# Optimization experiments

Measured on AMD Instinct MI355X. Metric: run time of the kernel, lower is better.

Reference implementation:

```python
import jax, jax.numpy as jnp
import numpy as np

B, S, H = 1, 2048, 1024
NQ, NKV, HD = 16, 8, 64
FF, E, TOPK = 2048, 4, 2
WINDOW = 512
CAP = 50.0
CLIP_L, CLIP_R = -0.03, 1.03
EPS = 1e-5
ROPE_BASE = 10000.0


def setup_inputs() -> dict:
    key = jax.random.key(0)
    ks = jax.random.split(key, 14)
    std = 0.02
    def nrm(k, shape):
        return jax.random.normal(k, shape, jnp.float32) * std
    return {
        'x': jax.random.normal(ks[0], (B, S, H), jnp.float32),
        'norm1_w': 1.0 + nrm(ks[1], (H,)),
        'wq': nrm(ks[2], (H, NQ * HD)),
        'wk': nrm(ks[3], (H, NKV * HD)),
        'wv': nrm(ks[4], (H, NKV * HD)),
        'wo': nrm(ks[5], (NQ * HD, H)),
        'qn_w': 1.0 + nrm(ks[6], (HD,)),
        'kn_w': 1.0 + nrm(ks[7], (HD,)),
        'norm2_w': 1.0 + nrm(ks[8], (H,)),
        'gate_w': nrm(ks[9], (H, E)),
        'w_gate': nrm(ks[10], (E, H, FF)),
        'w_up': nrm(ks[11], (E, H, FF)),
        'w_down': nrm(ks[12], (E, FF, H)),
    }


def _rms(x, w):
    return x * jax.lax.rsqrt(jnp.mean(x * x, axis=-1, keepdims=True) + EPS) * w


def _rope(t):
    # t: [B, S, N, D]
    D = t.shape[-1]
    half = D // 2
    inv = 1.0 / (ROPE_BASE ** (jnp.arange(half, dtype=jnp.float32) / half))
    ang = jnp.arange(t.shape[1], dtype=jnp.float32)[:, None] * inv  # [S, half]
    cos = jnp.cos(ang)[None, :, None, :]
    sin = jnp.sin(ang)[None, :, None, :]
    t1, t2 = t[..., :half], t[..., half:]
    return jnp.concatenate([t1 * cos - t2 * sin, t1 * sin + t2 * cos], axis=-1)


def reference(x, norm1_w, wq, wk, wv, wo, qn_w, kn_w, norm2_w, gate_w, w_gate, w_up, w_down):
    # --- self-attention block ---
    xn = _rms(x, norm1_w)
    q = (xn @ wq).reshape(B, S, NQ, HD)
    k = (xn @ wk).reshape(B, S, NKV, HD)
    v = (xn @ wv).reshape(B, S, NKV, HD)
    q = _rms(_rope(q), qn_w)  # RoPE then QK-norm over head_dim
    k = _rms(_rope(k), kn_w)
    rep = NQ // NKV
    k = jnp.repeat(k, rep, axis=2)  # GQA expand to NQ heads
    v = jnp.repeat(v, rep, axis=2)
    scale = 1.0 / np.sqrt(HD).astype(np.float32)
    scores = jnp.einsum('bqhd,bkhd->bhqk', q, k) * scale
    scores = CAP * jnp.tanh(scores / CAP)  # softmax capping (overrides temperature)
    i = jnp.arange(S)[:, None]
    j = jnp.arange(S)[None, :]
    allow = (j <= i) & (i - j < WINDOW)  # causal + sliding window
    scores = jnp.where(allow[None, None], scores, -jnp.inf)
    p = jax.nn.softmax(scores, axis=-1)
    p = jnp.clip((CLIP_R - CLIP_L) * p + CLIP_L, 0.0, 1.0)  # softmax clipping
    attn = jnp.einsum('bhqk,bkhd->bqhd', p, v).reshape(B, S, NQ * HD)
    h = x + attn @ wo
    # --- MoE gated-SiLU MLP block ---
    xn2 = _rms(h, norm2_w).reshape(B * S, H)
    probs = jax.nn.softmax(xn2 @ gate_w, axis=-1)
    topv, topi = jax.lax.top_k(probs, TOPK)
    topv = topv / jnp.sum(topv, axis=-1, keepdims=True)
    T = B * S
    wdense = jnp.zeros((T, E), jnp.float32).at[jnp.arange(T)[:, None], topi].add(topv)
    g = jnp.einsum('th,ehf->etf', xn2, w_gate)
    u = jnp.einsum('th,ehf->etf', xn2, w_up)
    y = jnp.einsum('etf,efh->eth', jax.nn.silu(g) * u, w_down)
    moe = jnp.einsum('eth,te->th', y, wdense)
    return h + moe.reshape(B, S, H)
```

## Files before the change

kernel.cpp:

```cpp
#include <hip/hip_runtime.h>
#include <hip/hip_bf16.h>
#include <math.h>

#define S_LEN   2048
#define H_DIM   1024
#define N_QH    16
#define N_KVH   8
#define HEADD   64
#define FF_DIM  2048
#define N_EXP   4
#define WIN     512
#define QB      16
#define SCS     596

typedef __attribute__((ext_vector_type(8))) short bf16x8;
typedef __attribute__((ext_vector_type(4))) float f32x4;

__device__ __forceinline__ short f2bf(float x) {
  unsigned u = __float_as_uint(x);
  u += 0x7fffu + ((u >> 16) & 1u);
  return (short)(u >> 16);
}
__device__ __forceinline__ float bf2f(short h) {
  return __uint_as_float((unsigned)(unsigned short)h << 16);
}
__device__ __forceinline__ unsigned pk2(short a, short b) {
  return (unsigned)(unsigned short)a | ((unsigned)(unsigned short)b << 16);
}
__device__ __forceinline__ int swz(int row, int col) {
  return row * 64 + (col ^ ((row & 7) << 3));
}

__global__ __launch_bounds__(256) void k_rope_tables(float* __restrict__ ct, float* __restrict__ st) {
  int i = blockIdx.x * 256 + threadIdx.x;
  int t = i >> 5, d = i & 31;
  double inv = 1.0 / pow(10000.0, (double)d / 32.0);
  double ang = (double)t * inv;
  ct[i] = (float)cos(ang);
  st[i] = (float)sin(ang);
}

template <int MODE>
__global__ __launch_bounds__(256) void k_rmsnorm(const float* __restrict__ x,
                                                 const float* __restrict__ w,
                                                 short* __restrict__ yh,
                                                 short* __restrict__ yl,
                                                 const float* __restrict__ gw,
                                                 float* __restrict__ wd) {
  int row = blockIdx.x;
  const float4 v = ((const float4*)(x + (long)row * H_DIM))[threadIdx.x];
  float ss = v.x * v.x + v.y * v.y + v.z * v.z + v.w * v.w;
  for (int off = 32; off; off >>= 1) ss += __shfl_xor(ss, off);
  __shared__ float red[4];
  if ((threadIdx.x & 63) == 0) red[threadIdx.x >> 6] = ss;
  __syncthreads();
  ss = red[0] + red[1] + red[2] + red[3];
  float r = (float)(1.0 / sqrt((double)ss * (1.0 / 1024.0) + 1e-5));
  const float4 wv = ((const float4*)w)[threadIdx.x];
  float4 o;
  o.x = v.x * r * wv.x; o.y = v.y * r * wv.y; o.z = v.z * r * wv.z; o.w = v.w * r * wv.w;
  if (MODE == 2) {
    short h0 = f2bf(o.x), h1 = f2bf(o.y), h2 = f2bf(o.z), h3 = f2bf(o.w);
    short l0 = f2bf(o.x - bf2f(h0)), l1 = f2bf(o.y - bf2f(h1));
    short l2 = f2bf(o.z - bf2f(h2)), l3 = f2bf(o.w - bf2f(h3));
    ((uint2*)(yh + (long)row * H_DIM))[threadIdx.x] = make_uint2(pk2(h0, h1), pk2(h2, h3));
    ((uint2*)(yl + (long)row * H_DIM))[threadIdx.x] = make_uint2(pk2(l0, l1), pk2(l2, l3));
  }
  if (MODE == 3) {
    ((uint2*)(yh + (long)row * H_DIM))[threadIdx.x] =
        make_uint2(pk2(f2bf(o.x), f2bf(o.y)), pk2(f2bf(o.z), f2bf(o.w)));
    int i0 = threadIdx.x * 4;
    float4 g0 = *(const float4*)&gw[(i0 + 0) * 4];
    float4 g1 = *(const float4*)&gw[(i0 + 1) * 4];
    float4 g2 = *(const float4*)&gw[(i0 + 2) * 4];
    float4 g3 = *(const float4*)&gw[(i0 + 3) * 4];
    float p0 = o.x * g0.x + o.y * g1.x + o.z * g2.x + o.w * g3.x;
    float p1 = o.x * g0.y + o.y * g1.y + o.z * g2.y + o.w * g3.y;
    float p2 = o.x * g0.z + o.y * g1.z + o.z * g2.z + o.w * g3.z;
    float p3 = o.x * g0.w + o.y * g1.w + o.z * g2.w + o.w * g3.w;
    for (int off = 32; off; off >>= 1) {
      p0 += __shfl_xor(p0, off); p1 += __shfl_xor(p1, off);
      p2 += __shfl_xor(p2, off); p3 += __shfl_xor(p3, off);
    }
    __shared__ float gred[4][4];
    int wid = threadIdx.x >> 6;
    if ((threadIdx.x & 63) == 0) { gred[wid][0] = p0; gred[wid][1] = p1; gred[wid][2] = p2; gred[wid][3] = p3; }
    __syncthreads();
    if (threadIdx.x == 0) {
      float l[4];
      for (int e = 0; e < 4; ++e) l[e] = gred[0][e] + gred[1][e] + gred[2][e] + gred[3][e];
      int i1 = 0;
      for (int e = 1; e < 4; ++e) if (l[e] > l[i1]) i1 = e;
      int i2 = -1;
      for (int e = 0; e < 4; ++e) { if (e == i1) continue; if (i2 < 0 || l[e] > l[i2]) i2 = e; }
      float e2 = expf(l[i2] - l[i1]);
      float w1 = 1.f / (1.f + e2);
      float ov[4] = {0.f, 0.f, 0.f, 0.f};
      ov[i1] = w1; ov[i2] = 1.f - w1;
      wd[row * 4 + 0] = ov[0]; wd[row * 4 + 1] = ov[1];
      wd[row * 4 + 2] = ov[2]; wd[row * 4 + 3] = ov[3];
    }
  }
}

__global__ __launch_bounds__(256) void k_tsplit(const float* __restrict__ in,
                                                short* __restrict__ oh,
                                                short* __restrict__ ol, int R, int C) {
  __shared__ float tile[32][33];
  int bx = blockIdx.x, by = blockIdx.y;
  int lx = threadIdx.x & 31, ly = threadIdx.x >> 5;
  int xc = bx * 32 + lx;
#pragma unroll
  for (int k = 0; k < 4; ++k) {
    int y = by * 32 + ly + k * 8;
    tile[ly + k * 8][lx] = in[(long)y * C + xc];
  }
  __syncthreads();
  int ox = by * 32 + lx;
#pragma unroll
  for (int k = 0; k < 4; ++k) {
    int oy = bx * 32 + ly + k * 8;
    float v = tile[lx][ly + k * 8];
    short hb = f2bf(v);
    short lb = f2bf(v - bf2f(hb));
    oh[(long)oy * R + ox] = hb;
    ol[(long)oy * R + ox] = lb;
  }
}

__global__ __launch_bounds__(256) void k_transpose_cast(const float* __restrict__ in,
                                                        short* __restrict__ out,
                                                        int R, int C) {
  __shared__ float tile[32][33];
  int bx = blockIdx.x, by = blockIdx.y;
  int lx = threadIdx.x & 31, ly = threadIdx.x >> 5;
  int x = bx * 32 + lx;
#pragma unroll
  for (int k = 0; k < 4; ++k) {
    int y = by * 32 + ly + k * 8;
    tile[ly + k * 8][lx] = in[(long)y * C + x];
  }
  __syncthreads();
  int ox = by * 32 + lx;
#pragma unroll
  for (int k = 0; k < 4; ++k) {
    int oy = bx * 32 + ly + k * 8;
    out[(long)oy * R + ox] = f2bf(tile[lx][ly + k * 8]);
  }
}

template <int ADD>
__global__ __launch_bounds__(256) void k_gemm_split(const short* __restrict__ Ah,
                                                    const short* __restrict__ Al,
                                                    const short* __restrict__ Bh,
                                                    const short* __restrict__ Bl,
                                                    const float* __restrict__ R,
                                                    float* __restrict__ C,
                                                    int K, int ldA, int ldB, int ldC) {
  __shared__ short AsH[128 * 64], AsL[128 * 64], BsH[128 * 64], BsL[128 * 64];
  const int r0 = blockIdx.x * 128, c0 = blockIdx.y * 128;
  const int tid = threadIdx.x;
  const int wid = tid >> 6, lane = tid & 63;
  const int wr = wid >> 1, wc = wid & 1;
  const int lr = lane & 15, lg = lane >> 4;
  f32x4 zero = {0.f, 0.f, 0.f, 0.f};
  f32x4 acc[4][4];
#pragma unroll
  for (int m = 0; m < 4; ++m)
#pragma unroll
    for (int n = 0; n < 4; ++n) acc[m][n] = zero;
  for (int k0 = 0; k0 < K; k0 += 64) {
#pragma unroll
    for (int it = 0; it < 4; ++it) {
      int flat = tid + it * 256;
      int row = flat >> 3, cb = (flat & 7) * 8;
      int d = swz(row, cb);
      *(uint4*)&AsH[d] = *(const uint4*)&Ah[(long)(r0 + row) * ldA + k0 + cb];
      *(uint4*)&AsL[d] = *(const uint4*)&Al[(long)(r0 + row) * ldA + k0 + cb];
      *(uint4*)&BsH[d] = *(const uint4*)&Bh[(long)(c0 + row) * ldB + k0 + cb];
      *(uint4*)&BsL[d] = *(const uint4*)&Bl[(long)(c0 + row) * ldB + k0 + cb];
    }
    __syncthreads();
#pragma unroll
    for (int kk = 0; kk < 64; kk += 32) {
      bf16x8 ah[4], al[4], bh[4], bl[4];
#pragma unroll
      for (int m = 0; m < 4; ++m) {
        int d = swz(wr * 64 + m * 16 + lr, kk + lg * 8);
        ah[m] = *(const bf16x8*)&AsH[d];
        al[m] = *(const bf16x8*)&AsL[d];
      }
#pragma unroll
      for (int n = 0; n < 4; ++n) {
        int d = swz(wc * 64 + n * 16 + lr, kk + lg * 8);
        bh[n] = *(const bf16x8*)&BsH[d];
        bl[n] = *(const bf16x8*)&BsL[d];
      }
#pragma unroll
      for (int m = 0; m < 4; ++m)
#pragma unroll
        for (int n = 0; n < 4; ++n) {
          acc[m][n] = __builtin_amdgcn_mfma_f32_16x16x32_bf16(ah[m], bh[n], acc[m][n], 0, 0, 0);
          acc[m][n] = __builtin_amdgcn_mfma_f32_16x16x32_bf16(ah[m], bl[n], acc[m][n], 0, 0, 0);
          acc[m][n] = __builtin_amdgcn_mfma_f32_16x16x32_bf16(al[m], bh[n], acc[m][n], 0, 0, 0);
        }
    }
    __syncthreads();
  }
#pragma unroll
  for (int m = 0; m < 4; ++m)
#pragma unroll
    for (int n = 0; n < 4; ++n) {
      int col = c0 + wc * 64 + n * 16 + lr;
#pragma unroll
      for (int r = 0; r < 4; ++r) {
        int row = r0 + wr * 64 + m * 16 + lg * 4 + r;
        float v = acc[m][n][r];
        if (ADD) v += R[(long)row * ldC + col];
        C[(long)row * ldC + col] = v;
      }
    }
}

__global__ __launch_bounds__(256) void k_rope_rms(float* __restrict__ qkv,
                                                  const float* __restrict__ qn_w,
                                                  const float* __restrict__ kn_w,
                                                  const float* __restrict__ ct,
                                                  const float* __restrict__ st) {
  int idx = blockIdx.x * 4 + (threadIdx.x >> 6);
  int lane = threadIdx.x & 63;
  int t = idx / 24, hh = idx - t * 24;
  long base; const float* w;
  if (hh < N_QH) { base = (long)t * 2048 + hh * HEADD;              w = qn_w; }
  else           { base = (long)t * 2048 + 1024 + (hh - N_QH) * HEADD; w = kn_w; }
  float x = qkv[base + lane];
  float partner = __shfl_xor(x, 32);
  int d = lane & 31;
  float cs = ct[t * 32 + d], sn = st[t * 32 + d];
  float r = x * cs + partner * ((lane < 32) ? -sn : sn);
  float ss = r * r;
  for (int off = 32; off; off >>= 1) ss += __shfl_xor(ss, off);
  float rr = (float)(1.0 / sqrt((double)ss * (1.0 / 64.0) + 1e-5));
  qkv[base + lane] = r * rr * w[lane];
}

__global__ __launch_bounds__(256) void k_kv_split(const float* __restrict__ qkv,
                                                  short* __restrict__ Kbh, short* __restrict__ Kbl,
                                                  short* __restrict__ Vth, short* __restrict__ Vtl) {
  const int kvh = blockIdx.y;
  const int jb = blockIdx.x * 64;
  const int tid = threadIdx.x;
  {
    int j = jb + (tid >> 2);
    int dq = (tid & 3) * 16;
    const float* kp = &qkv[(long)j * 2048 + 1024 + kvh * HEADD + dq];
    long ob = ((long)kvh * S_LEN + j) * HEADD + dq;
#pragma unroll
    for (int u4 = 0; u4 < 4; ++u4) {
      float4 f = *(const float4*)&kp[u4 * 4];
      short h0 = f2bf(f.x), h1 = f2bf(f.y), h2 = f2bf(f.z), h3 = f2bf(f.w);
      short l0 = f2bf(f.x - bf2f(h0)), l1 = f2bf(f.y - bf2f(h1));
      short l2 = f2bf(f.z - bf2f(h2)), l3 = f2bf(f.w - bf2f(h3));
      *(uint2*)&Kbh[ob + u4 * 4] = make_uint2(pk2(h0, h1), pk2(h2, h3));
      *(uint2*)&Kbl[ob + u4 * 4] = make_uint2(pk2(l0, l1), pk2(l2, l3));
    }
  }
  {
    int d = tid & 63;
    int j0 = jb + (tid >> 6) * 16;
    short hb[16], lb[16];
#pragma unroll
    for (int u = 0; u < 16; ++u) {
      float f = qkv[(long)(j0 + u) * 2048 + 1536 + kvh * HEADD + d];
      hb[u] = f2bf(f);
      lb[u] = f2bf(f - bf2f(hb[u]));
    }
    long ob = ((long)kvh * HEADD + d) * S_LEN + j0;
#pragma unroll
    for (int w = 0; w < 2; ++w) {
      uint4 oh, ol;
      oh.x = pk2(hb[w * 8 + 0], hb[w * 8 + 1]); oh.y = pk2(hb[w * 8 + 2], hb[w * 8 + 3]);
      oh.z = pk2(hb[w * 8 + 4], hb[w * 8 + 5]); oh.w = pk2(hb[w * 8 + 6], hb[w * 8 + 7]);
      ol.x = pk2(lb[w * 8 + 0], lb[w * 8 + 1]); ol.y = pk2(lb[w * 8 + 2], lb[w * 8 + 3]);
      ol.z = pk2(lb[w * 8 + 4], lb[w * 8 + 5]); ol.w = pk2(lb[w * 8 + 6], lb[w * 8 + 7]);
      *(uint4*)&Vth[ob + w * 8] = oh;
      *(uint4*)&Vtl[ob + w * 8] = ol;
    }
  }
}

__global__ __launch_bounds__(256) void k_attn2(const float* __restrict__ qkv,
                                               const short* __restrict__ Kbh,
                                               const short* __restrict__ Kbl,
                                               const short* __restrict__ Vth,
                                               const short* __restrict__ Vtl,
                                               short* __restrict__ attHi,
                                               short* __restrict__ attLo) {
  __shared__ float sc[QB][SCS];
  __shared__ float row_a[QB];
  const int i0 = blockIdx.x * QB;
  const int hq = blockIdx.y;
  const int kvh = hq >> 1;
  const int tid = threadIdx.x;
  const int wv = tid >> 6, lane = tid & 63;
  const int lr = lane & 15, lg = lane >> 4;
  const int jstart = (i0 >= WIN) ? ((i0 - (WIN - 1)) & ~63) : 0;
  const int nch = (i0 + QB - jstart + 63) >> 6;
  const int ncols = nch * 64;
  f32x4 zero = {0.f, 0.f, 0.f, 0.f};
  const short* Kh_p = Kbh + (long)kvh * S_LEN * HEADD;
  const short* Kl_p = Kbl + (long)kvh * S_LEN * HEADD;
  const short* Vh_p = Vth + (long)kvh * HEADD * S_LEN;
  const short* Vl_p = Vtl + (long)kvh * HEADD * S_LEN;

  bf16x8 qh[2], ql[2];
  {
    const float* qp = &qkv[(long)(i0 + lr) * 2048 + hq * HEADD];
#pragma unroll
    for (int kk = 0; kk < 2; ++kk) {
      float4 f0 = *(const float4*)&qp[kk * 32 + lg * 8];
      float4 f1 = *(const float4*)&qp[kk * 32 + lg * 8 + 4];
      float ff[8] = {f0.x, f0.y, f0.z, f0.w, f1.x, f1.y, f1.z, f1.w};
      bf16x8 h, l;
#pragma unroll
      for (int u = 0; u < 8; ++u) {
        short hb = f2bf(ff[u]);
        h[u] = hb; l[u] = f2bf(ff[u] - bf2f(hb));
      }
      qh[kk] = h; ql[kk] = l;
    }
  }

  for (int ch = 0; ch < nch; ++ch) {
    int jb = jstart + ch * 64;
    int jrow = jb + wv * 16 + lr;
    int jc = min(jrow, S_LEN - 1);
    f32x4 s = zero;
#pragma unroll
    for (int kk = 0; kk < 2; ++kk) {
      bf16x8 kh = *(const bf16x8*)&Kh_p[(long)jc * HEADD + kk * 32 + lg * 8];
      bf16x8 kl = *(const bf16x8*)&Kl_p[(long)jc * HEADD + kk * 32 + lg * 8];
      s = __builtin_amdgcn_mfma_f32_16x16x32_bf16(qh[kk], kh, s, 0, 0, 0);
      s = __builtin_amdgcn_mfma_f32_16x16x32_bf16(qh[kk], kl, s, 0, 0, 0);
      s = __builtin_amdgcn_mfma_f32_16x16x32_bf16(ql[kk], kh, s, 0, 0, 0);
    }
    int col = ch * 64 + wv * 16 + lr;
#pragma unroll
    for (int r = 0; r < 4; ++r) {
      int q = 4 * lg + r;
      int i = i0 + q;
      float v = s[r] * 0.125f;
      v = 50.f * tanhf(v * 0.02f);
      bool allow = (jrow <= i) && (i - jrow < WIN);
      sc[q][col] = allow ? v : -1e30f;
    }
  }
  __syncthreads();

  for (int r = wv * 4; r < wv * 4 + 4; ++r) {
    float mx = -1e30f;
    for (int n = lane; n < ncols; n += 64) mx = fmaxf(mx, sc[r][n]);
    for (int off = 32; off; off >>= 1) mx = fmaxf(mx, __shfl_xor(mx, off));
    float sum = 0.f;
    for (int n = lane; n < ncols; n += 64) {
      float p = expf(sc[r][n] - mx);
      sc[r][n] = p; sum += p;
    }
    for (int off = 32; off; off >>= 1) sum += __shfl_xor(sum, off);
    if (lane == 0) row_a[r] = 1.06f / sum;
  }
  __syncthreads();

  {
    int q = tid >> 4;
    float a = row_a[q];
    for (int n = (tid & 15); n < ncols; n += 16) {
      float e = sc[q][n];
      float p = fminf(fmaxf(fmaf(a, e, -0.03f), 0.f), 1.f);
      short ph = f2bf(p);
      short pl = f2bf(p - bf2f(ph));
      *(unsigned*)&sc[q][n] = pk2(ph, pl);
    }
  }
  __syncthreads();

  f32x4 oacc = zero;
  for (int ch = 0; ch < nch; ++ch) {
    int jb = jstart + ch * 64;
#pragma unroll
    for (int kk = 0; kk < 2; ++kk) {
      int js = jb + kk * 32 + lg * 8;
      int jcb = min(js, S_LEN - 8);
      const unsigned* pp = (const unsigned*)&sc[lr][ch * 64 + kk * 32 + lg * 8];
      uint4 w0 = *(const uint4*)&pp[0];
      uint4 w1 = *(const uint4*)&pp[4];
      bf16x8 pa, pb;
      pa[0] = (short)w0.x; pb[0] = (short)(w0.x >> 16);
      pa[1] = (short)w0.y; pb[1] = (short)(w0.y >> 16);
      pa[2] = (short)w0.z; pb[2] = (short)(w0.z >> 16);
      pa[3] = (short)w0.w; pb[3] = (short)(w0.w >> 16);
      pa[4] = (short)w1.x; pb[4] = (short)(w1.x >> 16);
      pa[5] = (short)w1.y; pb[5] = (short)(w1.y >> 16);
      pa[6] = (short)w1.z; pb[6] = (short)(w1.z >> 16);
      pa[7] = (short)w1.w; pb[7] = (short)(w1.w >> 16);
      bf16x8 vh = *(const bf16x8*)&Vh_p[(long)(wv * 16 + lr) * S_LEN + jcb];
      bf16x8 vl = *(const bf16x8*)&Vl_p[(long)(wv * 16 + lr) * S_LEN + jcb];
      oacc = __builtin_amdgcn_mfma_f32_16x16x32_bf16(pa, vh, oacc, 0, 0, 0);
      oacc = __builtin_amdgcn_mfma_f32_16x16x32_bf16(pa, vl, oacc, 0, 0, 0);
      oacc = __builtin_amdgcn_mfma_f32_16x16x32_bf16(pb, vh, oacc, 0, 0, 0);
    }
  }
#pragma unroll
  for (int r = 0; r < 4; ++r) {
    int q = 4 * lg + r;
    int d = wv * 16 + lr;
    long ob = (long)(i0 + q) * 1024 + hq * HEADD + d;
    float v = oacc[r];
    short hb = f2bf(v);
    attHi[ob] = hb;
    attLo[ob] = f2bf(v - bf2f(hb));
  }
}

template <int ATOMIC>
__global__ __launch_bounds__(256) void k_gemm_bf16(const short* __restrict__ A,
                                                   const short* __restrict__ Bt,
                                                   float* __restrict__ C,
                                                   int K, int ldA, int ldB, int ldC,
                                                   long sA, long sB, long sC) {
  __shared__ short As[128 * 64];
  __shared__ short Bs[128 * 64];
  const int e = blockIdx.z;
  A += (long)e * sA; Bt += (long)e * sB; C += (long)e * sC;
  const int r0 = blockIdx.x * 128, c0 = blockIdx.y * 128;
  const int tid = threadIdx.x;
  const int wid = tid >> 6, lane = tid & 63;
  const int wr = wid >> 1, wc = wid & 1;
  const int lr = lane & 15, lg = lane >> 4;
  f32x4 zero = {0.f, 0.f, 0.f, 0.f};
  f32x4 acc[4][4];
#pragma unroll
  for (int m = 0; m < 4; ++m)
#pragma unroll
    for (int n = 0; n < 4; ++n) acc[m][n] = zero;
  for (int k0 = 0; k0 < K; k0 += 64) {
#pragma unroll
    for (int it = 0; it < 4; ++it) {
      int flat = tid + it * 256;
      int row = flat >> 3, cb = (flat & 7) * 8;
      int d = swz(row, cb);
      *(uint4*)&As[d] = *(const uint4*)&A[(long)(r0 + row) * ldA + k0 + cb];
      *(uint4*)&Bs[d] = *(const uint4*)&Bt[(long)(c0 + row) * ldB + k0 + cb];
    }
    __syncthreads();
#pragma unroll
    for (int kk = 0; kk < 64; kk += 32) {
      bf16x8 af[4], bfr[4];
#pragma unroll
      for (int m = 0; m < 4; ++m) af[m] = *(const bf16x8*)&As[swz(wr * 64 + m * 16 + lr, kk + lg * 8)];
#pragma unroll
      for (int n = 0; n < 4; ++n) bfr[n] = *(const bf16x8*)&Bs[swz(wc * 64 + n * 16 + lr, kk + lg * 8)];
#pragma unroll
      for (int m = 0; m < 4; ++m)
#pragma unroll
        for (int n = 0; n < 4; ++n)
          acc[m][n] = __builtin_amdgcn_mfma_f32_16x16x32_bf16(af[m], bfr[n], acc[m][n], 0, 0, 0);
    }
    __syncthreads();
  }
#pragma unroll
  for (int m = 0; m < 4; ++m)
#pragma unroll
    for (int n = 0; n < 4; ++n) {
      int col = c0 + wc * 64 + n * 16 + lr;
#pragma unroll
      for (int r = 0; r < 4; ++r) {
        int row = r0 + wr * 64 + m * 16 + lg * 4 + r;
        float v = acc[m][n][r];
        if (ATOMIC) atomicAdd(&C[(long)row * ldC + col], v);
        else        C[(long)row * ldC + col] = v;
      }
    }
}

__global__ __launch_bounds__(256) void k_moe_act(const float* __restrict__ gu,
                                                 const float* __restrict__ wd,
                                                 short* __restrict__ aAll,
                                                 int e) {
  long i4 = (long)blockIdx.x * 256 + threadIdx.x;
  int t  = (int)(i4 >> 9);
  int f4 = (int)(i4 & 511);
  float wte = wd[t * 4 + e];
  float4 g = ((const float4*)gu)[(long)t * 1024 + f4];
  float4 u = ((const float4*)gu)[(long)t * 1024 + 512 + f4];
  float4 s;
  s.x = wte * u.x * g.x / (1.f + expf(-g.x));
  s.y = wte * u.y * g.y / (1.f + expf(-g.y));
  s.z = wte * u.z * g.z / (1.f + expf(-g.z));
  s.w = wte * u.w * g.w / (1.f + expf(-g.w));
  ((uint2*)(aAll + ((long)e << 22)))[i4] =
      make_uint2(pk2(f2bf(s.x), f2bf(s.y)), pk2(f2bf(s.z), f2bf(s.w)));
}

extern "C" void kernel_launch(void* const* d_in, const int* in_sizes, int n_in,
                              void* d_out, int out_size, void* d_ws, size_t ws_size,
                              hipStream_t stream) {
  const float* x       = (const float*)d_in[0];
  const float* norm1_w = (const float*)d_in[1];
  const float* wq      = (const float*)d_in[2];
  const float* wk      = (const float*)d_in[3];
  const float* wv      = (const float*)d_in[4];
  const float* wo      = (const float*)d_in[5];
  const float* qn_w    = (const float*)d_in[6];
  const float* kn_w    = (const float*)d_in[7];
  const float* norm2_w = (const float*)d_in[8];
  const float* gate_w  = (const float*)d_in[9];
  const float* w_gate  = (const float*)d_in[10];
  const float* w_up    = (const float*)d_in[11];
  const float* w_down  = (const float*)d_in[12];
  float* out = (float*)d_out;
  char* ws = (char*)d_ws;
  const unsigned long MB = 1ul << 20;

  float* ropeC = (float*)(ws + 0);
  float* ropeS = (float*)(ws + 256 * 1024);
  float* qkv   = (float*)(ws + 1 * MB);
  short* xnHi  = (short*)(ws + 17 * MB);
  short* xnLo  = (short*)(ws + 21 * MB);
  short* attHi = (short*)(ws + 25 * MB);
  short* attLo = (short*)(ws + 29 * MB);
  float* gu    = (float*)(ws + 1 * MB);
  short* qkvWh = (short*)(ws + 33 * MB);
  short* qkvWl = (short*)(ws + 37 * MB);
  short* woTh  = (short*)(ws + 41 * MB);
  short* woTl  = (short*)(ws + 43 * MB);
  float* h     = (float*)(ws + 45 * MB);
  short* guT   = (short*)(ws + 45 * MB);
  short* x2b   = (short*)(ws + 53 * MB);
  float* wd    = (float*)(ws + 57 * MB);
  short* dT    = (short*)(ws + 58 * MB);
  short* Kbh   = (short*)(ws + 58 * MB);
  short* Kbl   = (short*)(ws + 60 * MB);
  short* Vth   = (short*)(ws + 62 * MB);
  short* Vtl   = (short*)(ws + 64 * MB);
  short* aAll  = (short*)(ws + 74 * MB);

  k_rope_tables<<<256, 256, 0, stream>>>(ropeC, ropeS);
  k_rmsnorm<2><<<S_LEN, 256, 0, stream>>>(x, norm1_w, xnHi, xnLo, nullptr, nullptr);
  k_tsplit<<<dim3(32, 32), 256, 0, stream>>>(wq, qkvWh, qkvWl, 1024, 1024);
  k_tsplit<<<dim3(16, 32), 256, 0, stream>>>(wk, qkvWh + 1024 * 1024, qkvWl + 1024 * 1024, 1024, 512);
  k_tsplit<<<dim3(16, 32), 256, 0, stream>>>(wv, qkvWh + 1536 * 1024, qkvWl + 1536 * 1024, 1024, 512);
  k_tsplit<<<dim3(32, 32), 256, 0, stream>>>(wo, woTh, woTl, 1024, 1024);
  k_gemm_split<0><<<dim3(16, 16), 256, 0, stream>>>(xnHi, xnLo, qkvWh, qkvWl, nullptr, qkv,
                                                    1024, 1024, 1024, 2048);
  k_rope_rms<<<(S_LEN * 24) / 4, 256, 0, stream>>>(qkv, qn_w, kn_w, ropeC, ropeS);
  k_kv_split<<<dim3(S_LEN / 64, N_KVH), 256, 0, stream>>>(qkv, Kbh, Kbl, Vth, Vtl);
  k_attn2<<<dim3(S_LEN / QB, N_QH), 256, 0, stream>>>(qkv, Kbh, Kbl, Vth, Vtl, attHi, attLo);
  k_gemm_split<1><<<dim3(16, 8), 256, 0, stream>>>(attHi, attLo, woTh, woTl, x, h,
                                                   1024, 1024, 1024, 1024);
  k_rmsnorm<3><<<S_LEN, 256, 0, stream>>>(h, norm2_w, x2b, nullptr, gate_w, wd);
  hipMemcpyAsync(out, h, (size_t)S_LEN * H_DIM * sizeof(float), hipMemcpyDeviceToDevice, stream);
  for (int e = 0; e < N_EXP; ++e)
    k_transpose_cast<<<dim3(1024 / 32, 2048 / 32), 256, 0, stream>>>(
        w_down + (long)e * FF_DIM * H_DIM, dT + (long)e * H_DIM * FF_DIM, 2048, 1024);
  for (int e = 0; e < N_EXP; ++e) {
    k_transpose_cast<<<dim3(2048 / 32, 1024 / 32), 256, 0, stream>>>(
        w_gate + (long)e * H_DIM * FF_DIM, guT, 1024, 2048);
    k_transpose_cast<<<dim3(2048 / 32, 1024 / 32), 256, 0, stream>>>(
        w_up + (long)e * H_DIM * FF_DIM, guT + (long)FF_DIM * H_DIM, 1024, 2048);
    k_gemm_bf16<0><<<dim3(16, 32), 256, 0, stream>>>(x2b, guT, gu, 1024, 1024, 1024, 4096, 0, 0, 0);
    k_moe_act<<<4096, 256, 0, stream>>>(gu, wd, aAll, e);
  }
  k_gemm_bf16<1><<<dim3(16, 8, N_EXP), 256, 0, stream>>>(
      aAll, dT, out, 2048, 2048, 2048, 1024,
      (long)S_LEN * FF_DIM, (long)H_DIM * FF_DIM, 0);
}
```

Measured before the change: 579.7 us.

## Route MoE tokens sparsely to top-2 experts and use fast softcap/exp intrinsics

The MoE block previously ran dense GEMMs for every token through all four experts and weighted the results. A routing kernel now builds per-expert token lists with atomic counters, and the gate/up and down GEMMs gather only the assigned tokens, skipping empty tiles and scattering results with atomics. This roughly halves the MoE FLOPs, at the cost of a gather inside the A-tile load and nondeterministic token ordering. Separately, the attention tanh softcap is rewritten as an exp plus reciprocal, and expf is replaced by __expf and rcp intrinsics, trading a little precision for cheaper transcendentals.

```diff
diff --git a/kernel.cpp b/kernel.cpp
--- a/kernel.cpp
+++ b/kernel.cpp
@@ -27,6 +27,10 @@
 __device__ __forceinline__ unsigned pk2(short a, short b) {
   return (unsigned)(unsigned short)a | ((unsigned)(unsigned short)b << 16);
 }
+__device__ __forceinline__ float softcap(float s) {
+  float e = __expf(s * 0.04f);
+  return 50.f - 100.f * __builtin_amdgcn_rcpf(e + 1.f);
+}
 __device__ __forceinline__ int swz(int row, int col) {
   return row * 64 + (col ^ ((row & 7) << 3));
 }
@@ -46,7 +50,7 @@
                                                  short* __restrict__ yh,
                                                  short* __restrict__ yl,
                                                  const float* __restrict__ gw,
-                                                 float* __restrict__ wd) {
+                                                 float* __restrict__ route) {
   int row = blockIdx.x;
   const float4 v = ((const float4*)(x + (long)row * H_DIM))[threadIdx.x];
   float ss = v.x * v.x + v.y * v.y + v.z * v.z + v.w * v.w;
@@ -95,12 +99,22 @@
       for (int e = 0; e < 4; ++e) { if (e == i1) continue; if (i2 < 0 || l[e] > l[i2]) i2 = e; }
       float e2 = expf(l[i2] - l[i1]);
       float w1 = 1.f / (1.f + e2);
-      float ov[4] = {0.f, 0.f, 0.f, 0.f};
-      ov[i1] = w1; ov[i2] = 1.f - w1;
-      wd[row * 4 + 0] = ov[0]; wd[row * 4 + 1] = ov[1];
-      wd[row * 4 + 2] = ov[2]; wd[row * 4 + 3] = ov[3];
-    }
-  }
+      *(float4*)&route[row * 4] = make_float4((float)i1, (float)i2, w1, 1.f - w1);
+    }
+  }
+}
+
+__global__ __launch_bounds__(256) void k_route(const float* __restrict__ route,
+                                               int* __restrict__ idx,
+                                               float* __restrict__ wsl,
+                                               int* __restrict__ cnt) {
+  int t = blockIdx.x * 256 + threadIdx.x;
+  float4 rt = *(const float4*)&route[t * 4];
+  int e1 = (int)rt.x, e2 = (int)rt.y;
+  int s1 = atomicAdd(&cnt[e1], 1);
+  idx[e1 * S_LEN + s1] = t; wsl[e1 * S_LEN + s1] = rt.z;
+  int s2 = atomicAdd(&cnt[e2], 1);
+  idx[e2 * S_LEN + s2] = t; wsl[e2 * S_LEN + s2] = rt.w;
 }
 
 __global__ __launch_bounds__(256) void k_tsplit(const float* __restrict__ in,
@@ -349,8 +363,7 @@
     for (int r = 0; r < 4; ++r) {
       int q = 4 * lg + r;
       int i = i0 + q;
-      float v = s[r] * 0.125f;
-      v = 50.f * tanhf(v * 0.02f);
+      float v = softcap(s[r] * 0.125f);
       bool allow = (jrow <= i) && (i - jrow < WIN);
       sc[q][col] = allow ? v : -1e30f;
     }
@@ -363,7 +376,7 @@
     for (int off = 32; off; off >>= 1) mx = fmaxf(mx, __shfl_xor(mx, off));
     float sum = 0.f;
     for (int n = lane; n < ncols; n += 64) {
-      float p = expf(sc[r][n] - mx);
+      float p = __expf(sc[r][n] - mx);
       sc[r][n] = p; sum += p;
     }
     for (int off = 32; off; off >>= 1) sum += __shfl_xor(sum, off);
@@ -422,17 +435,17 @@
   }
 }
 
-template <int ATOMIC>
-__global__ __launch_bounds__(256) void k_gemm_bf16(const short* __restrict__ A,
+__global__ __launch_bounds__(256) void k_gemm_moe1(const short* __restrict__ A,
                                                    const short* __restrict__ Bt,
                                                    float* __restrict__ C,
-                                                   int K, int ldA, int ldB, int ldC,
-                                                   long sA, long sB, long sC) {
+                                                   const int* __restrict__ idx,
+                                                   const int* __restrict__ cnt) {
+  const int n = *cnt;
+  const int r0 = blockIdx.x * 128;
+  if (r0 >= n) return;
   __shared__ short As[128 * 64];
   __shared__ short Bs[128 * 64];
-  const int e = blockIdx.z;
-  A += (long)e * sA; Bt += (long)e * sB; C += (long)e * sC;
-  const int r0 = blockIdx.x * 128, c0 = blockIdx.y * 128;
+  const int c0 = blockIdx.y * 128;
   const int tid = threadIdx.x;
   const int wid = tid >> 6, lane = tid & 63;
   const int wr = wid >> 1, wc = wid & 1;
@@ -442,15 +455,82 @@
 #pragma unroll
   for (int m = 0; m < 4; ++m)
 #pragma unroll
-    for (int n = 0; n < 4; ++n) acc[m][n] = zero;
-  for (int k0 = 0; k0 < K; k0 += 64) {
+    for (int nn = 0; nn < 4; ++nn) acc[m][nn] = zero;
+  int tokRow[1];
+  for (int k0 = 0; k0 < 1024; k0 += 64) {
+#pragma unroll
+    for (int it = 0; it < 4; ++it) {
+      int flat = tid + it * 256;
+      int row = flat >> 3, cb = (flat & 7) * 8;
+      int slot = r0 + row;
+      int tok = idx[min(slot, n - 1)];
+      int d = swz(row, cb);
+      *(uint4*)&As[d] = *(const uint4*)&A[(long)tok * 1024 + k0 + cb];
+      *(uint4*)&Bs[d] = *(const uint4*)&Bt[(long)(c0 + row) * 1024 + k0 + cb];
+    }
+    (void)tokRow;
+    __syncthreads();
+#pragma unroll
+    for (int kk = 0; kk < 64; kk += 32) {
+      bf16x8 af[4], bfr[4];
+#pragma unroll
+      for (int m = 0; m < 4; ++m) af[m] = *(const bf16x8*)&As[swz(wr * 64 + m * 16 + lr, kk + lg * 8)];
+#pragma unroll
+      for (int nn = 0; nn < 4; ++nn) bfr[nn] = *(const bf16x8*)&Bs[swz(wc * 64 + nn * 16 + lr, kk + lg * 8)];
+#pragma unroll
+      for (int m = 0; m < 4; ++m)
+#pragma unroll
+        for (int nn = 0; nn < 4; ++nn)
+          acc[m][nn] = __builtin_amdgcn_mfma_f32_16x16x32_bf16(af[m], bfr[nn], acc[m][nn], 0, 0, 0);
+    }
+    __syncthreads();
+  }
+#pragma unroll
+  for (int m = 0; m < 4; ++m)
+#pragma unroll
+    for (int nn = 0; nn < 4; ++nn) {
+      int col = c0 + wc * 64 + nn * 16 + lr;
+#pragma unroll
+      for (int r = 0; r < 4; ++r) {
+        int row = r0 + wr * 64 + m * 16 + lg * 4 + r;
+        C[(long)row * 4096 + col] = acc[m][nn][r];
+      }
+    }
+}
+
+__global__ __launch_bounds__(256) void k_gemm_moe2(const short* __restrict__ aAll,
+                                                   const short* __restrict__ dT,
+                                                   float* __restrict__ out,
+                                                   const int* __restrict__ idx,
+                                                   const int* __restrict__ cnt) {
+  const int e = blockIdx.z;
+  const int n = cnt[e];
+  const int r0 = blockIdx.x * 128;
+  if (r0 >= n) return;
+  __shared__ short As[128 * 64];
+  __shared__ short Bs[128 * 64];
+  const short* A = aAll + ((long)e << 22);
+  const short* Bt = dT + (long)e * H_DIM * FF_DIM;
+  const int* eidx = idx + e * S_LEN;
+  const int c0 = blockIdx.y * 128;
+  const int tid = threadIdx.x;
+  const int wid = tid >> 6, lane = tid & 63;
+  const int wr = wid >> 1, wc = wid & 1;
+  const int lr = lane & 15, lg = lane >> 4;
+  f32x4 zero = {0.f, 0.f, 0.f, 0.f};
+  f32x4 acc[4][4];
+#pragma unroll
+  for (int m = 0; m < 4; ++m)
+#pragma unroll
+    for (int nn = 0; nn < 4; ++nn) acc[m][nn] = zero;
+  for (int k0 = 0; k0 < 2048; k0 += 64) {
 #pragma unroll
     for (int it = 0; it < 4; ++it) {
       int flat = tid + it * 256;
       int row = flat >> 3, cb = (flat & 7) * 8;
       int d = swz(row, cb);
-      *(uint4*)&As[d] = *(const uint4*)&A[(long)(r0 + row) * ldA + k0 + cb];
-      *(uint4*)&Bs[d] = *(const uint4*)&Bt[(long)(c0 + row) * ldB + k0 + cb];
+      *(uint4*)&As[d] = *(const uint4*)&A[(long)(r0 + row) * 2048 + k0 + cb];
+      *(uint4*)&Bs[d] = *(const uint4*)&Bt[(long)(c0 + row) * 2048 + k0 + cb];
     }
     __syncthreads();
 #pragma unroll
@@ -459,45 +539,48 @@
 #pragma unroll
       for (int m = 0; m < 4; ++m) af[m] = *(const bf16x8*)&As[swz(wr * 64 + m * 16 + lr, kk + lg * 8)];
 #pragma unroll
-      for (int n = 0; n < 4; ++n) bfr[n] = *(const bf16x8*)&Bs[swz(wc * 64 + n * 16 + lr, kk + lg * 8)];
+      for (int nn = 0; nn < 4; ++nn) bfr[nn] = *(const bf16x8*)&Bs[swz(wc * 64 + nn * 16 + lr, kk + lg * 8)];
 #pragma unroll
       for (int m = 0; m < 4; ++m)
 #pragma unroll
-        for (int n = 0; n < 4; ++n)
-          acc[m][n] = __builtin_amdgcn_mfma_f32_16x16x32_bf16(af[m], bfr[n], acc[m][n], 0, 0, 0);
+        for (int nn = 0; nn < 4; ++nn)
+          acc[m][nn] = __builtin_amdgcn_mfma_f32_16x16x32_bf16(af[m], bfr[nn], acc[m][nn], 0, 0, 0);
     }
     __syncthreads();
   }
 #pragma unroll
   for (int m = 0; m < 4; ++m)
 #pragma unroll
-    for (int n = 0; n < 4; ++n) {
-      int col = c0 + wc * 64 + n * 16 + lr;
+    for (int nn = 0; nn < 4; ++nn) {
+      int col = c0 + wc * 64 + nn * 16 + lr;
 #pragma unroll
       for (int r = 0; r < 4; ++r) {
-        int row = r0 + wr * 64 + m * 16 + lg * 4 + r;
-        float v = acc[m][n][r];
-        if (ATOMIC) atomicAdd(&C[(long)row * ldC + col], v);
-        else        C[(long)row * ldC + col] = v;
+        int slot = r0 + wr * 64 + m * 16 + lg * 4 + r;
+        if (slot < n) {
+          int tok = eidx[slot];
+          atomicAdd(&out[(long)tok * 1024 + col], acc[m][nn][r]);
+        }
       }
     }
 }
 
 __global__ __launch_bounds__(256) void k_moe_act(const float* __restrict__ gu,
-                                                 const float* __restrict__ wd,
+                                                 const float* __restrict__ wsl,
+                                                 const int* __restrict__ cnt,
                                                  short* __restrict__ aAll,
                                                  int e) {
   long i4 = (long)blockIdx.x * 256 + threadIdx.x;
-  int t  = (int)(i4 >> 9);
+  int slot = (int)(i4 >> 9);
+  if (slot >= cnt[e]) return;
   int f4 = (int)(i4 & 511);
-  float wte = wd[t * 4 + e];
-  float4 g = ((const float4*)gu)[(long)t * 1024 + f4];
-  float4 u = ((const float4*)gu)[(long)t * 1024 + 512 + f4];
+  float w = wsl[e * S_LEN + slot];
+  float4 g = ((const float4*)gu)[(long)slot * 1024 + f4];
+  float4 u = ((const float4*)gu)[(long)slot * 1024 + 512 + f4];
   float4 s;
-  s.x = wte * u.x * g.x / (1.f + expf(-g.x));
-  s.y = wte * u.y * g.y / (1.f + expf(-g.y));
-  s.z = wte * u.z * g.z / (1.f + expf(-g.z));
-  s.w = wte * u.w * g.w / (1.f + expf(-g.w));
+  s.x = w * u.x * g.x * __builtin_amdgcn_rcpf(1.f + __expf(-g.x));
+  s.y = w * u.y * g.y * __builtin_amdgcn_rcpf(1.f + __expf(-g.y));
+  s.z = w * u.z * g.z * __builtin_amdgcn_rcpf(1.f + __expf(-g.z));
+  s.w = w * u.w * g.w * __builtin_amdgcn_rcpf(1.f + __expf(-g.w));
   ((uint2*)(aAll + ((long)e << 22)))[i4] =
       make_uint2(pk2(f2bf(s.x), f2bf(s.y)), pk2(f2bf(s.z), f2bf(s.w)));
 }
@@ -521,9 +604,10 @@
   float* out = (float*)d_out;
   char* ws = (char*)d_ws;
   const unsigned long MB = 1ul << 20;
+  const unsigned long KB = 1ul << 10;
 
   float* ropeC = (float*)(ws + 0);
-  float* ropeS = (float*)(ws + 256 * 1024);
+  float* ropeS = (float*)(ws + 256 * KB);
   float* qkv   = (float*)(ws + 1 * MB);
   short* xnHi  = (short*)(ws + 17 * MB);
   short* xnLo  = (short*)(ws + 21 * MB);
@@ -537,7 +621,10 @@
   float* h     = (float*)(ws + 45 * MB);
   short* guT   = (short*)(ws + 45 * MB);
   short* x2b   = (short*)(ws + 53 * MB);
-  float* wd    = (float*)(ws + 57 * MB);
+  float* route = (float*)(ws + 57 * MB);
+  int*   idx   = (int*)  (ws + 57 * MB + 32 * KB);
+  float* wsl   = (float*)(ws + 57 * MB + 64 * KB);
+  int*   cnt   = (int*)  (ws + 57 * MB + 96 * KB);
   short* dT    = (short*)(ws + 58 * MB);
   short* Kbh   = (short*)(ws + 58 * MB);
   short* Kbl   = (short*)(ws + 60 * MB);
@@ -545,6 +632,7 @@
   short* Vtl   = (short*)(ws + 64 * MB);
   short* aAll  = (short*)(ws + 74 * MB);
 
+  hipMemsetAsync(cnt, 0, 16, stream);
   k_rope_tables<<<256, 256, 0, stream>>>(ropeC, ropeS);
   k_rmsnorm<2><<<S_LEN, 256, 0, stream>>>(x, norm1_w, xnHi, xnLo, nullptr, nullptr);
   k_tsplit<<<dim3(32, 32), 256, 0, stream>>>(wq, qkvWh, qkvWl, 1024, 1024);
@@ -558,7 +646,8 @@
   k_attn2<<<dim3(S_LEN / QB, N_QH), 256, 0, stream>>>(qkv, Kbh, Kbl, Vth, Vtl, attHi, attLo);
   k_gemm_split<1><<<dim3(16, 8), 256, 0, stream>>>(attHi, attLo, woTh, woTl, x, h,
                                                    1024, 1024, 1024, 1024);
-  k_rmsnorm<3><<<S_LEN, 256, 0, stream>>>(h, norm2_w, x2b, nullptr, gate_w, wd);
+  k_rmsnorm<3><<<S_LEN, 256, 0, stream>>>(h, norm2_w, x2b, nullptr, gate_w, route);
+  k_route<<<8, 256, 0, stream>>>(route, idx, wsl, cnt);
   hipMemcpyAsync(out, h, (size_t)S_LEN * H_DIM * sizeof(float), hipMemcpyDeviceToDevice, stream);
   for (int e = 0; e < N_EXP; ++e)
     k_transpose_cast<<<dim3(1024 / 32, 2048 / 32), 256, 0, stream>>>(
@@ -568,10 +657,8 @@
         w_gate + (long)e * H_DIM * FF_DIM, guT, 1024, 2048);
     k_transpose_cast<<<dim3(2048 / 32, 1024 / 32), 256, 0, stream>>>(
         w_up + (long)e * H_DIM * FF_DIM, guT + (long)FF_DIM * H_DIM, 1024, 2048);
-    k_gemm_bf16<0><<<dim3(16, 32), 256, 0, stream>>>(x2b, guT, gu, 1024, 1024, 1024, 4096, 0, 0, 0);
-    k_moe_act<<<4096, 256, 0, stream>>>(gu, wd, aAll, e);
-  }
-  k_gemm_bf16<1><<<dim3(16, 8, N_EXP), 256, 0, stream>>>(
-      aAll, dT, out, 2048, 2048, 2048, 1024,
-      (long)S_LEN * FF_DIM, (long)H_DIM * FF_DIM, 0);
-}
+    k_gemm_moe1<<<dim3(16, 32), 256, 0, stream>>>(x2b, guT, gu, idx + e * S_LEN, cnt + e);
+    k_moe_act<<<4096, 256, 0, stream>>>(gu, wsl, cnt, aAll, e);
+  }
+  k_gemm_moe2<<<dim3(16, 8, N_EXP), 256, 0, stream>>>(aAll, dT, out, idx, cnt);
+}
```

Measured after the change: 591.9 us. 1.02x slower.
